# Optimization experiments

Hardware: AMD Instinct MI355X
Metric: run time of the kernel (lower is better)

The kernel has to match this reference:

```python
import jax, jax.numpy as jnp
import numpy as np

HIDDEN = 2048
NUM_HEADS = 16
NUM_KV_HEADS = 4
HEAD_DIM = HIDDEN // NUM_HEADS  # 128
WINDOW = 512
THETA = 10000.0
BATCH = 4
SEQ = 2048
NEG = -1e30


def _apply_rope(x, pos, theta):
    # x: [T, H, D] with interleaved even/odd rotation, matching the torch strided slicing
    half = x.shape[-1] // 2
    inv_freq = 1.0 / (theta ** (jnp.arange(half, dtype=jnp.float32) / half))
    ang = pos.astype(jnp.float32)[:, None] * inv_freq[None, :]          # [T, half]
    cos = jnp.cos(ang)[:, None, :]                                       # [T, 1, half]
    sin = jnp.sin(ang)[:, None, :]
    xe = x[..., 0::2].astype(jnp.float32)
    xo = x[..., 1::2].astype(jnp.float32)
    re = xe * cos - xo * sin
    ro = xe * sin + xo * cos
    out = jnp.stack([re, ro], axis=-1).reshape(x.shape)                  # re-interleave
    return out.astype(x.dtype)


def setup_inputs() -> dict:
    key = jax.random.key(0)
    ks = jax.random.split(key, 5)
    sc = 1.0 / np.sqrt(HIDDEN)
    hidden_states = jax.random.normal(ks[0], (BATCH * SEQ, HIDDEN), dtype=jnp.float32)
    q_w = jax.random.normal(ks[1], (HIDDEN, NUM_HEADS * HEAD_DIM), dtype=jnp.float32) * sc
    k_w = jax.random.normal(ks[2], (HIDDEN, NUM_KV_HEADS * HEAD_DIM), dtype=jnp.float32) * sc
    v_w = jax.random.normal(ks[3], (HIDDEN, NUM_KV_HEADS * HEAD_DIM), dtype=jnp.float32) * sc
    o_w = jax.random.normal(ks[4], (HIDDEN, HIDDEN), dtype=jnp.float32) * sc
    position_ids = jnp.tile(jnp.arange(SEQ, dtype=jnp.int32), BATCH)     # restart per sequence
    cu_seqlens = jnp.arange(BATCH + 1, dtype=jnp.int32) * SEQ
    return {
        "hidden_states": hidden_states, "q_w": q_w, "k_w": k_w, "v_w": v_w, "o_w": o_w,
        "position_ids": position_ids, "cu_seqlens": cu_seqlens, "max_seq_len": SEQ,
    }


def reference(hidden_states, q_w, k_w, v_w, o_w, position_ids, cu_seqlens, max_seq_len):
    T = hidden_states.shape[0]
    B = cu_seqlens.shape[0] - 1
    S = T // B  # equal-length packing
    groups = NUM_HEADS // NUM_KV_HEADS

    q = (hidden_states @ q_w).reshape(T, NUM_HEADS, HEAD_DIM)
    k = (hidden_states @ k_w).reshape(T, NUM_KV_HEADS, HEAD_DIM)
    v = (hidden_states @ v_w).reshape(T, NUM_KV_HEADS, HEAD_DIM)

    q = _apply_rope(q, position_ids, THETA)
    k = _apply_rope(k, position_ids, THETA)

    q = q.reshape(B, S, NUM_HEADS, HEAD_DIM)
    k = k.reshape(B, S, NUM_KV_HEADS, HEAD_DIM)
    v = v.reshape(B, S, NUM_KV_HEADS, HEAD_DIM)
    # GQA: expand kv heads to query heads
    k = jnp.repeat(k, groups, axis=2)   # [B, S, H, D]
    v = jnp.repeat(v, groups, axis=2)

    scale = 1.0 / np.sqrt(HEAD_DIM)
    scores = jnp.einsum('bqhd,bkhd->bhqk', q, k) * scale  # [B, H, S, S]

    pos = position_ids.reshape(B, S)
    pq = pos[:, None, :, None]
    pk = pos[:, None, None, :]
    # causal + sliding window (flash window_size=(WINDOW, 0) semantics): q-k in [0, WINDOW]
    allowed = (pk <= pq) & ((pq - pk) <= WINDOW)
    scores = jnp.where(allowed, scores, NEG)

    probs = jax.nn.softmax(scores, axis=-1)
    attn = jnp.einsum('bhqk,bkhd->bqhd', probs, v)        # [B, S, H, D]
    attn = attn.reshape(T, HIDDEN)
    return attn @ o_w
```

## Files before the change

### kernel.cpp

```cpp
#include <hip/hip_runtime.h>
#include <hip/hip_bf16.h>
#include <cstdint>
#include <cstddef>

typedef __bf16 bf16;
typedef __bf16 bf16x2 __attribute__((ext_vector_type(2)));
typedef __bf16 bf16x8 __attribute__((ext_vector_type(8)));
typedef float  f32x4  __attribute__((ext_vector_type(4)));

#define HIDDEN 2048
#define NHEADS 16
#define NKV    4
#define HD     128
#define WINDOW 512

__device__ __forceinline__ void gld16(const void* g, void* s) {
  __builtin_amdgcn_global_load_lds((const __attribute__((address_space(1))) void*)g,
                                   (__attribute__((address_space(3))) void*)s, 16, 0, 0);
}

__device__ __forceinline__ f32x4 mfma16(bf16x8 a, bf16x8 b, f32x4 c) {
  return __builtin_amdgcn_mfma_f32_16x16x32_bf16(a, b, c, 0, 0, 0);
}

__device__ __forceinline__ void barrier_raw() {
  asm volatile("" ::: "memory");
  __builtin_amdgcn_s_barrier();
  asm volatile("" ::: "memory");
}

__global__ __launch_bounds__(256) void cast_f32_bf16(const float* __restrict__ in,
                                                     bf16* __restrict__ out, int n4) {
  int i = blockIdx.x * 256 + threadIdx.x;
  if (i >= n4) return;
  f32x4 v = *(const f32x4*)(in + (size_t)i * 4);
  bf16x2 a, b;
  a[0] = (bf16)v[0]; a[1] = (bf16)v[1];
  b[0] = (bf16)v[2]; b[1] = (bf16)v[3];
  *(bf16x2*)(out + (size_t)i * 4)     = a;
  *(bf16x2*)(out + (size_t)i * 4 + 2) = b;
}

__global__ __launch_bounds__(256) void transpose_cast(const float* __restrict__ in,
                                                      bf16* __restrict__ out, int R, int C) {
  __shared__ float tile[32][33];
  int c0 = blockIdx.x * 32, r0 = blockIdx.y * 32;
  int tx = threadIdx.x, ty = threadIdx.y;
  #pragma unroll
  for (int i = 0; i < 4; ++i)
    tile[ty + i * 8][tx] = in[(size_t)(r0 + ty + i * 8) * C + c0 + tx];
  __syncthreads();
  #pragma unroll
  for (int i = 0; i < 4; ++i)
    out[(size_t)(c0 + ty + i * 8) * R + r0 + tx] = (bf16)tile[tx][ty + i * 8];
}

__device__ __forceinline__ void stage128x32(const bf16* __restrict__ A,
                                            const bf16* __restrict__ Bt,
                                            bf16* sA, bf16* sB,
                                            int m0, int n0, int K, int kt, int tid) {
  int wbase = tid & ~63;
  #pragma unroll
  for (int r = 0; r < 2; ++r) {
    int e = (r * 256 + tid) * 8;
    int row = e >> 5, col = e & 31;
    gld16(A  + (size_t)(m0 + row) * K + (size_t)kt * 32 + col,
          sA + (size_t)(r * 256 + wbase) * 8);
    gld16(Bt + (size_t)(n0 + row) * K + (size_t)kt * 32 + col,
          sB + (size_t)(r * 256 + wbase) * 8);
  }
}

__global__ __launch_bounds__(256) void gemm_bt(const bf16* __restrict__ A,
                                               const bf16* __restrict__ Bt,
                                               void* __restrict__ Cv,
                                               bf16* __restrict__ Vtout,
                                               int M, int N, int K, int outMode) {
  __shared__ bf16 sA[2][128 * 32];
  __shared__ bf16 sB[2][128 * 32];
  int nb = N >> 7;
  int bm = (int)blockIdx.x / nb, bn = (int)blockIdx.x % nb;
  int m0 = bm << 7, n0 = bn << 7;
  int tid = threadIdx.x;
  int lane = tid & 63, w = tid >> 6;
  int li = lane & 15, g = lane >> 4, g8 = g * 8;
  int wm = w >> 1, wn = w & 1;
  f32x4 acc[4][4] = {};
  int NT = K >> 5;

  stage128x32(A, Bt, sA[0], sB[0], m0, n0, K, 0, tid);
  __syncthreads();
  for (int kt = 0; kt < NT; ++kt) {
    int cur = kt & 1;
    if (kt + 1 < NT)
      stage128x32(A, Bt, sA[cur ^ 1], sB[cur ^ 1], m0, n0, K, kt + 1, tid);
    bf16x8 af[4], bv[4];
    #pragma unroll
    for (int mt = 0; mt < 4; ++mt)
      af[mt] = *(const bf16x8*)&sA[cur][(wm * 64 + mt * 16 + li) * 32 + g8];
    #pragma unroll
    for (int nt = 0; nt < 4; ++nt)
      bv[nt] = *(const bf16x8*)&sB[cur][(wn * 64 + nt * 16 + li) * 32 + g8];
    #pragma unroll
    for (int mt = 0; mt < 4; ++mt)
      #pragma unroll
      for (int nt = 0; nt < 4; ++nt)
        acc[mt][nt] = mfma16(af[mt], bv[nt], acc[mt][nt]);
    __syncthreads();
  }
  #pragma unroll
  for (int mt = 0; mt < 4; ++mt)
    #pragma unroll
    for (int nt = 0; nt < 4; ++nt)
      #pragma unroll
      for (int j = 0; j < 4; ++j) {
        int row = m0 + wm * 64 + mt * 16 + g * 4 + j;
        int col = n0 + wn * 64 + nt * 16 + li;
        float v = acc[mt][nt][j];
        if (outMode == 0)      ((bf16*)Cv)[(size_t)row * N + col] = (bf16)v;
        else if (outMode == 1) ((bf16*)Cv)[(size_t)col * M + row] = (bf16)v;
        else if (outMode == 2) ((float*)Cv)[(size_t)row * N + col] = v;
        else {
          if (col < 512) ((bf16*)Cv)[(size_t)row * 512 + col] = (bf16)v;
          else           Vtout[(size_t)(col - 512) * M + row] = (bf16)v;
        }
      }
}

template<int RSP>
__device__ __forceinline__ void stage_quad(const bf16* __restrict__ G,
                                           bf16* __restrict__ sbuf,
                                           int grow0, int K, int k0, int half, int tid) {
  int w = tid >> 6, lane = tid & 63;
  int rl = lane >> 3;
  int col = ((lane & 7) ^ rl) * 8;
  #pragma unroll
  for (int r = 0; r < 2; ++r) {
    int lr0 = r * 64 + w * 8;
    int row0 = (lr0 & (RSP - 1)) + half * RSP + (lr0 / RSP) * 2 * RSP;
    gld16(G + (size_t)(grow0 + row0 + rl) * K + k0 + col,
          sbuf + row0 * 64);
  }
}

__global__ __launch_bounds__(512, 2) void gemm256(const bf16* __restrict__ A,
                                                  const bf16* __restrict__ Bt,
                                                  void* __restrict__ Cv,
                                                  int M, int N, int K, int outMode) {
  __shared__ bf16 sA[2][256 * 64];
  __shared__ bf16 sB[2][256 * 64];
  int nb = N >> 8;
  int cpx = (int)gridDim.x >> 3;
  int bid = (int)blockIdx.x;
  int swzb = (bid & 7) * cpx + (bid >> 3);
  int bm = swzb / nb, bn = swzb % nb;
  int m0 = bm << 8, n0 = bn << 8;
  int tid = threadIdx.x, lane = tid & 63, w = tid >> 6;
  int li = lane & 15, g = lane >> 4;
  int wm = w >> 2, wn = w & 3;
  int swz = (li & 7);

  f32x4 acc[8][4] = {};
  bf16x8 af[4][2];
  bf16x8 bv[2][2][2];

  int NT = K >> 6;

  stage_quad<64>(A,  sA[0], m0, K, 0, 0, tid);
  stage_quad<32>(Bt, sB[0], n0, K, 0, 0, tid);
  stage_quad<32>(Bt, sB[0], n0, K, 0, 1, tid);
  stage_quad<64>(A,  sA[0], m0, K, 0, 1, tid);

#define VMW(n) asm volatile("s_waitcnt vmcnt(" #n ")" ::: "memory")
#define SBAR() __builtin_amdgcn_sched_barrier(0)
#define LGKM(n) { asm volatile("s_waitcnt lgkmcnt(" #n ")" ::: "memory"); \
  __builtin_amdgcn_sched_barrier(0); }
#define LOAD_A256(mh) { _Pragma("unroll") for (int mf = 0; mf < 4; ++mf) \
  _Pragma("unroll") for (int ks = 0; ks < 2; ++ks) { \
    int row = wm * 128 + (mh) * 64 + mf * 16 + li; \
    af[mf][ks] = *(const bf16x8*)&sA[cur][row * 64 + ((ks * 4 + g) ^ swz) * 8]; } }
#define LOAD_B256(nh) { _Pragma("unroll") for (int nf = 0; nf < 2; ++nf) \
  _Pragma("unroll") for (int ks = 0; ks < 2; ++ks) { \
    int row = wn * 64 + (nh) * 32 + nf * 16 + li; \
    bv[nh][nf][ks] = *(const bf16x8*)&sB[cur][row * 64 + ((ks * 4 + g) ^ swz) * 8]; } }
#define MFMA_PH(mh, nh) { \
  __builtin_amdgcn_s_setprio(1); \
  _Pragma("unroll") for (int mf = 0; mf < 4; ++mf) \
  _Pragma("unroll") for (int nf = 0; nf < 2; ++nf) \
  _Pragma("unroll") for (int ks = 0; ks < 2; ++ks) \
    acc[(mh) * 4 + mf][(nh) * 2 + nf] = \
      mfma16(af[mf][ks], bv[nh][nf][ks], acc[(mh) * 4 + mf][(nh) * 2 + nf]); \
  __builtin_amdgcn_s_setprio(0); }

  int cur = 0;
  for (int t = 0; t < NT; ++t) {
    int nxt = cur ^ 1;
    bool pre = (t + 1 < NT);
    int k1 = (t + 1) << 6;
    VMW(0);
    barrier_raw();
    if (pre) stage_quad<64>(A, sA[nxt], m0, K, k1, 0, tid);
    LOAD_A256(0); LOAD_B256(0);
    SBAR();
    LOAD_B256(1);
    if (pre) stage_quad<32>(Bt, sB[nxt], n0, K, k1, 0, tid);
    LGKM(4);
    MFMA_PH(0, 0);
    if (pre) stage_quad<32>(Bt, sB[nxt], n0, K, k1, 1, tid);
    LGKM(0);
    MFMA_PH(0, 1);
    LOAD_A256(1);
    if (pre) stage_quad<64>(A, sA[nxt], m0, K, k1, 1, tid);
    LGKM(0);
    MFMA_PH(1, 1);
    MFMA_PH(1, 0);
    cur = nxt;
  }
#undef VMW
#undef SBAR
#undef LGKM
#undef LOAD_A256
#undef LOAD_B256
#undef MFMA_PH

  #pragma unroll
  for (int mi = 0; mi < 8; ++mi)
    #pragma unroll
    for (int ni = 0; ni < 4; ++ni)
      #pragma unroll
      for (int j = 0; j < 4; ++j) {
        int row = m0 + wm * 128 + mi * 16 + g * 4 + j;
        int col = n0 + wn * 64 + ni * 16 + li;
        float v = acc[mi][ni][j];
        if (outMode == 2) ((float*)Cv)[(size_t)row * N + col] = v;
        else              ((bf16*)Cv)[(size_t)row * N + col] = (bf16)v;
      }
}

__global__ __launch_bounds__(256) void rope_kernel(bf16* __restrict__ X,
                                                   const int* __restrict__ pos,
                                                   int T, int heads) {
  int idx = blockIdx.x * 256 + threadIdx.x;
  int total = T * heads * 64;
  if (idx >= total) return;
  int i = idx & 63;
  int rest = idx >> 6;
  int hh = rest % heads;
  int t = rest / heads;
  float inv = expf((float)i * (-9.210340371976184f / 64.0f));
  float ang = (float)pos[t] * inv;
  float s, c;
  sincosf(ang, &s, &c);
  bf16* p = X + ((size_t)t * heads + hh) * HD + 2 * i;
  bf16x2 xv = *(const bf16x2*)p;
  float xe = (float)xv[0], xo = (float)xv[1];
  bf16x2 r;
  r[0] = (bf16)(xe * c - xo * s);
  r[1] = (bf16)(xe * s + xo * c);
  *(bf16x2*)p = r;
}

__global__ __launch_bounds__(512) void attn_kernel(const bf16* __restrict__ Q,
                                                   const bf16* __restrict__ Kb,
                                                   const bf16* __restrict__ Vt,
                                                   const int* __restrict__ pos,
                                                   const int* __restrict__ cu,
                                                   bf16* __restrict__ O, int T, int B) {
  __shared__ bf16 sK[32 * 128];
  __shared__ bf16 sVt2[64 * 64];
  __shared__ bf16 sP[8][16 * 40];
  int bid = blockIdx.x;
  int kvh = bid & (NKV - 1);
  int q0 = (bid >> 2) * 64;
  int tid = threadIdx.x, lane = tid & 63, w = tid >> 6;
  int hh = w & 3, rh = w >> 2;
  int h = kvh * 4 + hh;
  int li = lane & 15, g = lane >> 4, g8 = g * 8;
  int rb0 = q0 + rh * 32;

  int seq_start = 0, seq_end = T;
  for (int b = 0; b < B; ++b) {
    int a = cu[b], e = cu[b + 1];
    if (q0 >= a && q0 < e) { seq_start = a; seq_end = e; }
  }

  bf16x8 qf[2][4];
  #pragma unroll
  for (int grp = 0; grp < 2; ++grp)
    #pragma unroll
    for (int kd = 0; kd < 4; ++kd)
      qf[grp][kd] = *(const bf16x8*)(Q + (size_t)(rb0 + grp * 16 + li) * HIDDEN
                                     + h * HD + kd * 32 + g8);

  int pq[2][4], pmin[2], pmax[2];
  #pragma unroll
  for (int grp = 0; grp < 2; ++grp) {
    #pragma unroll
    for (int j = 0; j < 4; ++j) pq[grp][j] = pos[rb0 + grp * 16 + g * 4 + j];
    pmin[grp] = pos[rb0 + grp * 16];
    pmax[grp] = pos[rb0 + grp * 16 + 15];
  }

  float lsum[2][4] = {};
  f32x4 acc[2][8] = {};
  int kstart = q0 - WINDOW;
  if (kstart < seq_start) kstart = seq_start;
  int kend = q0 + 64;
  if (kend > seq_end) kend = seq_end;
  const float scale = 0.08838834764831845f;

  for (int kb = kstart; kb < kend; kb += 32) {
    int wbase = (tid & ~63) * 8;
    {
      int n = tid;
      int krow = n >> 4, kc = (n & 15) ^ (krow & 7);
      gld16(Kb + (size_t)(kb + krow) * (NKV * HD) + kvh * HD + kc * 8, sK + wbase);
      int vr = n >> 3, vc = (n & 7) ^ (vr & 7);
      int vd = 2 * vr + (vc >> 2), vkey = (vc & 3) * 8;
      gld16(Vt + (size_t)(kvh * HD + vd) * T + kb + vkey, sVt2 + wbase);
    }
    __syncthreads();

    int pkf = pos[kb], pkl = pos[kb + 31];
    int pk0 = pos[kb + li], pk1 = pos[kb + 16 + li];
    #pragma unroll
    for (int grp = 0; grp < 2; ++grp) {
      if (pkf > pmax[grp] || pkl < pmin[grp] - WINDOW) continue;
      f32x4 s0v = {0.f, 0.f, 0.f, 0.f}, s1v = {0.f, 0.f, 0.f, 0.f};
      #pragma unroll
      for (int kd = 0; kd < 4; ++kd) {
        int c0 = (kd * 4 + g) ^ (li & 7);
        bf16x8 b0 = *(const bf16x8*)&sK[li * 128 + c0 * 8];
        bf16x8 b1 = *(const bf16x8*)&sK[(16 + li) * 128 + c0 * 8];
        s0v = mfma16(qf[grp][kd], b0, s0v);
        s1v = mfma16(qf[grp][kd], b1, s1v);
      }
      bool interior = (pkl <= pmin[grp]) && (pmax[grp] - pkf <= WINDOW);
      if (interior) {
        #pragma unroll
        for (int j = 0; j < 4; ++j) {
          float p0 = __expf(s0v[j] * scale);
          float p1 = __expf(s1v[j] * scale);
          lsum[grp][j] += p0 + p1;
          sP[w][(g * 4 + j) * 40 + li]      = (bf16)p0;
          sP[w][(g * 4 + j) * 40 + 16 + li] = (bf16)p1;
        }
      } else {
        #pragma unroll
        for (int j = 0; j < 4; ++j) {
          int d0 = pq[grp][j] - pk0, d1 = pq[grp][j] - pk1;
          float p0 = (d0 >= 0 && d0 <= WINDOW) ? __expf(s0v[j] * scale) : 0.f;
          float p1 = (d1 >= 0 && d1 <= WINDOW) ? __expf(s1v[j] * scale) : 0.f;
          lsum[grp][j] += p0 + p1;
          sP[w][(g * 4 + j) * 40 + li]      = (bf16)p0;
          sP[w][(g * 4 + j) * 40 + 16 + li] = (bf16)p1;
        }
      }
      bf16x8 pa = *(const bf16x8*)&sP[w][li * 40 + g8];
      #pragma unroll
      for (int dt = 0; dt < 8; ++dt) {
        int d = dt * 16 + li;
        int vr2 = d >> 1;
        int vc2 = ((d & 1) * 4 + g) ^ (vr2 & 7);
        bf16x8 vf = *(const bf16x8*)&sVt2[vr2 * 64 + vc2 * 8];
        acc[grp][dt] = mfma16(pa, vf, acc[grp][dt]);
      }
    }
    __syncthreads();
  }

  #pragma unroll
  for (int grp = 0; grp < 2; ++grp)
    #pragma unroll
    for (int j = 0; j < 4; ++j) {
      float rs = lsum[grp][j];
      rs += __shfl_xor(rs, 1);
      rs += __shfl_xor(rs, 2);
      rs += __shfl_xor(rs, 4);
      rs += __shfl_xor(rs, 8);
      float invl = 1.0f / rs;
      size_t base = (size_t)(rb0 + grp * 16 + g * 4 + j) * HIDDEN + h * HD;
      #pragma unroll
      for (int dt = 0; dt < 8; ++dt)
        O[base + dt * 16 + li] = (bf16)(acc[grp][dt][j] * invl);
    }
}

extern "C" void kernel_launch(void* const* d_in, const int* in_sizes, int n_in,
                              void* d_out, int out_size, void* d_ws, size_t ws_size,
                              hipStream_t stream) {
  const float* X  = (const float*)d_in[0];
  const float* qw = (const float*)d_in[1];
  const float* kw = (const float*)d_in[2];
  const float* vw = (const float*)d_in[3];
  const float* ow = (const float*)d_in[4];
  const int* pos = (const int*)d_in[5];
  const int* cu  = (const int*)d_in[6];
  int T = in_sizes[0] / HIDDEN;
  int B = in_sizes[6] - 1;
  float* out = (float*)d_out;

  bf16* ws = (bf16*)d_ws;
  size_t off = 0;
  bf16* Xb    = ws + off; off += (size_t)T * HIDDEN;
  bf16* Qb    = ws + off; off += (size_t)T * HIDDEN;
  bf16* Kb    = ws + off; off += (size_t)T * (NKV * HD);
  bf16* Vt    = ws + off; off += (size_t)T * (NKV * HD);
  bf16* qwT   = ws + off; off += (size_t)HIDDEN * HIDDEN;
  bf16* kvwT  = ws + off; off += (size_t)1024 * HIDDEN;
  bf16* owT   = ws + off; off += (size_t)HIDDEN * HIDDEN;

  cast_f32_bf16<<<(T * HIDDEN / 4 + 255) / 256, 256, 0, stream>>>(X, Xb, T * HIDDEN / 4);

  dim3 tb(32, 8);
  transpose_cast<<<dim3(HIDDEN / 32, HIDDEN / 32), tb, 0, stream>>>(qw, qwT, HIDDEN, HIDDEN);
  transpose_cast<<<dim3(512 / 32, HIDDEN / 32), tb, 0, stream>>>(kw, kvwT, HIDDEN, 512);
  transpose_cast<<<dim3(512 / 32, HIDDEN / 32), tb, 0, stream>>>(vw, kvwT + (size_t)512 * HIDDEN, HIDDEN, 512);
  transpose_cast<<<dim3(HIDDEN / 32, HIDDEN / 32), tb, 0, stream>>>(ow, owT, HIDDEN, HIDDEN);

  gemm256<<<(T / 256) * (HIDDEN / 256), 512, 0, stream>>>(Xb, qwT, Qb, T, HIDDEN, HIDDEN, 0);
  gemm_bt<<<(T / 128) * (1024 / 128), 256, 0, stream>>>(Xb, kvwT, Kb, Vt, T, 1024, HIDDEN, 3);

  rope_kernel<<<(T * NHEADS * 64 + 255) / 256, 256, 0, stream>>>(Qb, pos, T, NHEADS);
  rope_kernel<<<(T * NKV * 64 + 255) / 256, 256, 0, stream>>>(Kb, pos, T, NKV);

  attn_kernel<<<(T / 64) * NKV, 512, 0, stream>>>(Qb, Kb, Vt, pos, cu, Qb, T, B);

  gemm256<<<(T / 256) * (HIDDEN / 256), 512, 0, stream>>>(Qb, owT, out, T, HIDDEN, HIDDEN, 2);
}
```

Measured before the change: 347.9 us.

## Double-buffer K/V tiles in attention kernel with async prefetch

```diff
diff --git a/kernel.cpp b/kernel.cpp
--- a/kernel.cpp
+++ b/kernel.cpp
@@ -266,8 +266,8 @@
                                                    const int* __restrict__ pos,
                                                    const int* __restrict__ cu,
                                                    bf16* __restrict__ O, int T, int B) {
-  __shared__ bf16 sK[32 * 128];
-  __shared__ bf16 sVt2[64 * 64];
+  __shared__ bf16 sK[2][32 * 128];
+  __shared__ bf16 sVt2[2][64 * 64];
   __shared__ bf16 sP[8][16 * 40];
   int bid = blockIdx.x;
   int kvh = bid & (NKV - 1);
@@ -308,18 +308,28 @@
   int kend = q0 + 64;
   if (kend > seq_end) kend = seq_end;
   const float scale = 0.08838834764831845f;
-
-  for (int kb = kstart; kb < kend; kb += 32) {
-    int wbase = (tid & ~63) * 8;
-    {
-      int n = tid;
-      int krow = n >> 4, kc = (n & 15) ^ (krow & 7);
-      gld16(Kb + (size_t)(kb + krow) * (NKV * HD) + kvh * HD + kc * 8, sK + wbase);
-      int vr = n >> 3, vc = (n & 7) ^ (vr & 7);
-      int vd = 2 * vr + (vc >> 2), vkey = (vc & 3) * 8;
-      gld16(Vt + (size_t)(kvh * HD + vd) * T + kb + vkey, sVt2 + wbase);
-    }
-    __syncthreads();
+  int nt = (kend - kstart) >> 5;
+
+  int krow = tid >> 4, kc = (tid & 15) ^ (krow & 7);
+  int vr = tid >> 3, vc = (tid & 7) ^ (vr & 7);
+  int vd = 2 * vr + (vc >> 2), vkey = (vc & 3) * 8;
+  int wbase = (tid & ~63) * 8;
+
+#define STAGE(kb_, buf_) { \
+  gld16(Kb + (size_t)((kb_) + krow) * (NKV * HD) + kvh * HD + kc * 8, \
+        &sK[buf_][wbase]); \
+  gld16(Vt + (size_t)(kvh * HD + vd) * T + (kb_) + vkey, \
+        &sVt2[buf_][wbase]); }
+#define VMW(n) asm volatile("s_waitcnt vmcnt(" #n ")" ::: "memory")
+
+  STAGE(kstart, 0);
+  for (int t = 0; t < nt; ++t) {
+    int kb = kstart + t * 32;
+    int cur = t & 1;
+    bool pre = (t + 1 < nt);
+    if (pre) { STAGE(kb + 32, cur ^ 1); VMW(2); }
+    else     { VMW(0); }
+    barrier_raw();
 
     int pkf = pos[kb], pkl = pos[kb + 31];
     int pk0 = pos[kb + li], pk1 = pos[kb + 16 + li];
@@ -330,8 +340,8 @@
       #pragma unroll
       for (int kd = 0; kd < 4; ++kd) {
         int c0 = (kd * 4 + g) ^ (li & 7);
-        bf16x8 b0 = *(const bf16x8*)&sK[li * 128 + c0 * 8];
-        bf16x8 b1 = *(const bf16x8*)&sK[(16 + li) * 128 + c0 * 8];
+        bf16x8 b0 = *(const bf16x8*)&sK[cur][li * 128 + c0 * 8];
+        bf16x8 b1 = *(const bf16x8*)&sK[cur][(16 + li) * 128 + c0 * 8];
         s0v = mfma16(qf[grp][kd], b0, s0v);
         s1v = mfma16(qf[grp][kd], b1, s1v);
       }
@@ -362,12 +372,14 @@
         int d = dt * 16 + li;
         int vr2 = d >> 1;
         int vc2 = ((d & 1) * 4 + g) ^ (vr2 & 7);
-        bf16x8 vf = *(const bf16x8*)&sVt2[vr2 * 64 + vc2 * 8];
+        bf16x8 vf = *(const bf16x8*)&sVt2[cur][vr2 * 64 + vc2 * 8];
         acc[grp][dt] = mfma16(pa, vf, acc[grp][dt]);
       }
     }
-    __syncthreads();
-  }
+    barrier_raw();
+  }
+#undef STAGE
+#undef VMW
 
   #pragma unroll
   for (int grp = 0; grp < 2; ++grp)
```

Measured after the change: 335.7 us. -3.5%, faster.
